# Kernel optimization log

Hardware: AMD Instinct MI355X
Metric: run time of the kernel (lower is better)

Reference implementation:

```python
import jax, jax.numpy as jnp
import numpy as np

B, T, N, D = 32, 50, 100, 4
E = N * (N - 1)
N_IN, N_HID, N_OUT = T * D, 256, 4


def _mlp(x, w1, b1, w2, b2):
    # Linear -> ReLU -> (dropout=0) -> Linear
    return jax.nn.relu(x @ w1 + b1) @ w2 + b2


def setup_inputs() -> dict:
    key = jax.random.key(0)
    ks = jax.random.split(key, 12)
    # fully-connected directed graph, no self loops
    idx = np.array([(i, j) for i in range(N) for j in range(N) if i != j], dtype=np.int64)
    recv, sendr = idx[:, 0], idx[:, 1]
    rec = jnp.asarray(np.eye(N, dtype=np.float32)[recv])    # [E, N]
    send = jnp.asarray(np.eye(N, dtype=np.float32)[sendr])  # [E, N]

    def lin(k, fan_in, fan_out):
        kw, kb = jax.random.split(k)
        w = jax.random.normal(kw, (fan_in, fan_out), jnp.float32) * 0.02
        b = jax.random.normal(kb, (fan_out,), jnp.float32) * 0.02
        return w, b

    x = jax.random.normal(ks[0], (B, T, N, D), jnp.float32)
    w1a, b1a = lin(ks[1], N_IN, N_HID)
    w1b, b1b = lin(ks[2], N_HID, N_HID)
    w2a, b2a = lin(ks[3], 2 * N_HID, N_HID)
    w2b, b2b = lin(ks[4], N_HID, N_HID)
    w3a, b3a = lin(ks[5], N_HID, N_HID)
    w3b, b3b = lin(ks[6], N_HID, N_HID)
    w4a, b4a = lin(ks[7], 3 * N_HID, N_HID)
    w4b, b4b = lin(ks[8], N_HID, N_HID)
    wo, bo = lin(ks[9], N_HID, N_OUT)
    return {"x": x, "rec": rec, "send": send,
            "w1a": w1a, "b1a": b1a, "w1b": w1b, "b1b": b1b,
            "w2a": w2a, "b2a": b2a, "w2b": w2b, "b2b": b2b,
            "w3a": w3a, "b3a": b3a, "w3b": w3b, "b3b": b3b,
            "w4a": w4a, "b4a": b4a, "w4b": w4b, "b4b": b4b,
            "wo": wo, "bo": bo}


def reference(x, rec, send,
              w1a, b1a, w1b, b1b,
              w2a, b2a, w2b, b2b,
              w3a, b3a, w3b, b3b,
              w4a, b4a, w4b, b4b,
              wo, bo):
    # [B, T, N, D] -> [B, N, T*D]
    h = jnp.transpose(x, (0, 2, 1, 3)).reshape(x.shape[0], x.shape[2], -1)
    h = _mlp(h, w1a, b1a, w1b, b1b)                       # [B, N, H]
    # v2e: gather receiver/sender node states to edges
    e = jnp.concatenate([jnp.einsum('en,bnh->beh', rec, h),
                         jnp.einsum('en,bnh->beh', send, h)], axis=2)  # [B, E, 2H]
    e = _mlp(e, w2a, b2a, w2b, b2b)                       # [B, E, H]
    x_skip = e
    # e2v: scatter edges back to nodes, normalize by n_nodes
    v = jnp.einsum('en,beh->bnh', rec, e) / e.shape[-2] * (e.shape[-2] / rec.shape[1])
    v = jnp.einsum('en,beh->bnh', rec, e) / rec.shape[1]  # incoming / incoming.size(1)=N
    v = _mlp(v, w3a, b3a, w3b, b3b)                       # [B, N, H]
    e2 = jnp.concatenate([jnp.einsum('en,bnh->beh', rec, v),
                          jnp.einsum('en,bnh->beh', send, v)], axis=2)  # [B, E, 2H]
    e2 = jnp.concatenate([e2, x_skip], axis=2)            # [B, E, 3H]
    e2 = _mlp(e2, w4a, b4a, w4b, b4b)                     # [B, E, H]
    return e2 @ wo + bo                                   # [B, E, n_out]
```

## Files before the change

kernel.cpp:

```cpp
#include <hip/hip_runtime.h>
#include <hip/hip_bf16.h>
#include <stdint.h>


typedef __attribute__((ext_vector_type(8))) short short8;
typedef __attribute__((ext_vector_type(4))) float float4v;
typedef __attribute__((ext_vector_type(4))) unsigned short ushort4v;

__device__ inline float bf2f(unsigned short u) {
    union { unsigned int i; float f; } v; v.i = ((unsigned int)u) << 16; return v.f;
}

#if __has_builtin(__builtin_amdgcn_cvt_pk_bf16_f32)
typedef __attribute__((ext_vector_type(2))) __bf16 bf16x2;
__device__ inline unsigned int f2bf_pk(float a, float b) {
    union { bf16x2 v; unsigned int u; } c;
    c.v = __builtin_amdgcn_cvt_pk_bf16_f32(a, b);
    return c.u;
}
__device__ inline unsigned short f2bf(float f) {
    return (unsigned short)(f2bf_pk(f, f) & 0xFFFFu);
}
#else
__device__ inline unsigned short f2bf(float f) {
    union { float f; unsigned int i; } v; v.f = f;
    unsigned int i = v.i;
    return (unsigned short)((i + 0x7FFFu + ((i >> 16) & 1u)) >> 16);
}
__device__ inline unsigned int f2bf_pk(float a, float b) {
    return (unsigned int)f2bf(a) | ((unsigned int)f2bf(b) << 16);
}
#endif

__global__ __launch_bounds__(256) void prep_kernel(
        const float* __restrict__ x,
        const float* __restrict__ w1a, const float* __restrict__ w1b,
        const float* __restrict__ w2a, const float* __restrict__ w2b,
        const float* __restrict__ w3a, const float* __restrict__ w3b,
        const float* __restrict__ w4a, const float* __restrict__ b4a,
        const float* __restrict__ w4b, const float* __restrict__ b4b,
        const float* __restrict__ wo,  const float* __restrict__ bo,
        const float* __restrict__ b2b,
        unsigned short* __restrict__ Wp1a, unsigned short* __restrict__ Wp1b,
        unsigned short* __restrict__ Wp2r, unsigned short* __restrict__ Wp2s,
        unsigned short* __restrict__ Wp2b, unsigned short* __restrict__ Wp3a,
        unsigned short* __restrict__ Wp3b, unsigned short* __restrict__ Wp4r,
        unsigned short* __restrict__ Wp4s, unsigned short* __restrict__ Wpz,
        unsigned short* __restrict__ Wfp, float* __restrict__ bfv,
        float* __restrict__ b4ap, float* __restrict__ b2bs,
        unsigned short* __restrict__ hin) {
    int bx = blockIdx.x;
    int tid = threadIdx.x;
    if (bx < 2272) {
        const float* W; unsigned short* Wp; int Kin; int b0;
        if      (bx <  224) { W = w1a;             Wp = Wp1a; Kin = 200; b0 = 0;    }
        else if (bx <  480) { W = w1b;             Wp = Wp1b; Kin = 256; b0 = 224;  }
        else if (bx <  736) { W = w2a;             Wp = Wp2r; Kin = 256; b0 = 480;  }
        else if (bx <  992) { W = w2a + 256 * 256; Wp = Wp2s; Kin = 256; b0 = 736;  }
        else if (bx < 1248) { W = w2b;             Wp = Wp2b; Kin = 256; b0 = 992;  }
        else if (bx < 1504) { W = w3a;             Wp = Wp3a; Kin = 256; b0 = 1248; }
        else if (bx < 1760) { W = w3b;             Wp = Wp3b; Kin = 256; b0 = 1504; }
        else if (bx < 2016) { W = w4a;             Wp = Wp4r; Kin = 256; b0 = 1760; }
        else                { W = w4a + 256 * 256; Wp = Wp4s; Kin = 256; b0 = 2016; }
        int idx = (bx - b0) * 256 + tid;
        int k = idx >> 8, n = idx & 255;
        unsigned short v = (k < Kin) ? f2bf(W[k * 256 + n]) : (unsigned short)0;
        Wp[((size_t)(k >> 5) * 256 + n) * 32 + (k & 31)] = v;
    } else if (bx < 2528) {
        int k = bx - 2272, c = tid;
        float s = 0.f;
        for (int t = 0; t < 256; ++t)
            s += w2b[k * 256 + t] * w4a[(size_t)(512 + t) * 256 + c];
        Wpz[((size_t)(k >> 5) * 256 + c) * 32 + (k & 31)] = f2bf(s);
    } else if (bx < 2530) {
        int k = tid;
        if (bx == 2528) {
            float a[4] = {0.f, 0.f, 0.f, 0.f};
            for (int c = 0; c < 256; ++c) {
                float wv = w4b[k * 256 + c];
                #pragma unroll
                for (int o = 0; o < 4; ++o) a[o] += wv * wo[c * 4 + o];
            }
            #pragma unroll
            for (int n = 0; n < 16; ++n)
                Wfp[(size_t)(k >> 5) * 512 + n * 32 + (k & 31)] =
                    (n < 4) ? f2bf(a[n]) : (unsigned short)0;
            if (k < 4) {
                float s = bo[k];
                for (int c = 0; c < 256; ++c) s += b4b[c] * wo[c * 4 + k];
                bfv[k] = s;
            }
        } else {
            float s = b4a[k];
            for (int t = 0; t < 256; ++t)
                s += b2b[t] * w4a[(size_t)(512 + t) * 256 + k];
            b4ap[k] = s;
            b2bs[k] = 0.99f * b2b[k];
        }
    } else {
        int idx = (bx - 2530) * 256 + tid;
        if (idx < 3200 * 224) {
            int row = idx / 224;
            int c = idx - row * 224;
            int b = row / 100, n = row - b * 100;
            unsigned short v = 0;
            if (c < 200) {
                int t = c >> 2, d = c & 3;
                v = f2bf(x[(((size_t)(b * 50 + t)) * 100 + n) * 4 + d]);
            }
            hin[(size_t)row * 224 + c] = v;
        }
    }
}

__global__ __launch_bounds__(256) void node_fusedA_kernel(
        const unsigned short* __restrict__ hin,
        const unsigned short* __restrict__ Wp1a, const float* __restrict__ b1a,
        const unsigned short* __restrict__ Wp1b, const float* __restrict__ b1b,
        const unsigned short* __restrict__ Wp2r, const float* __restrict__ b2a,
        const unsigned short* __restrict__ Wp2s,
        unsigned short* __restrict__ U, unsigned short* __restrict__ Hs) {
    __shared__ __align__(16) unsigned short t1s[16 * 264];
    __shared__ __align__(16) unsigned short hs2[16 * 264];
    const int m0 = blockIdx.x * 16;
    const int tid  = threadIdx.x;
    const int wave = tid >> 6;
    const int lane = tid & 63;
    const int l15  = lane & 15;
    const int quad = lane >> 4;
    const int n0   = wave * 64;
    const int koff = quad * 8;

    {
        float4v acc[4];
        #pragma unroll
        for (int ni = 0; ni < 4; ++ni) acc[ni] = (float4v)(0.0f);
        for (int kb = 0; kb < 7; ++kb) {
            short8 af = *(const short8*)(hin + (size_t)(m0 + l15) * 224 + kb * 32 + koff);
            short8 bf[4];
            #pragma unroll
            for (int ni = 0; ni < 4; ++ni)
                bf[ni] = *(const short8*)(Wp1a + ((size_t)kb * 256 + n0 + ni * 16 + l15) * 32 + koff);
            #pragma unroll
            for (int ni = 0; ni < 4; ++ni)
                acc[ni] = __builtin_amdgcn_mfma_f32_16x16x32_bf16(af, bf[ni], acc[ni], 0, 0, 0);
        }
        #pragma unroll
        for (int ni = 0; ni < 4; ++ni) {
            int col = n0 + ni * 16 + l15;
            float bv = b1a[col];
            #pragma unroll
            for (int r = 0; r < 4; ++r) {
                float v = acc[ni][r] + bv;
                v = v > 0.f ? v : 0.f;
                t1s[(quad * 4 + r) * 264 + col] = f2bf(v);
            }
        }
    }
    __syncthreads();

    {
        float4v acc[4];
        #pragma unroll
        for (int ni = 0; ni < 4; ++ni) acc[ni] = (float4v)(0.0f);
        for (int kb = 0; kb < 8; ++kb) {
            short8 af = *(const short8*)(&t1s[l15 * 264 + kb * 32 + koff]);
            short8 bf[4];
            #pragma unroll
            for (int ni = 0; ni < 4; ++ni)
                bf[ni] = *(const short8*)(Wp1b + ((size_t)kb * 256 + n0 + ni * 16 + l15) * 32 + koff);
            #pragma unroll
            for (int ni = 0; ni < 4; ++ni)
                acc[ni] = __builtin_amdgcn_mfma_f32_16x16x32_bf16(af, bf[ni], acc[ni], 0, 0, 0);
        }
        #pragma unroll
        for (int ni = 0; ni < 4; ++ni) {
            int col = n0 + ni * 16 + l15;
            float bv = b1b[col];
            #pragma unroll
            for (int r = 0; r < 4; ++r)
                hs2[(quad * 4 + r) * 264 + col] = f2bf(acc[ni][r] + bv);
        }
    }
    __syncthreads();

    {
        float4v aU[4], aH[4];
        #pragma unroll
        for (int ni = 0; ni < 4; ++ni) { aU[ni] = (float4v)(0.0f); aH[ni] = (float4v)(0.0f); }
        for (int kb = 0; kb < 8; ++kb) {
            short8 af = *(const short8*)(&hs2[l15 * 264 + kb * 32 + koff]);
            #pragma unroll
            for (int ni = 0; ni < 4; ++ni) {
                short8 bu = *(const short8*)(Wp2r + ((size_t)kb * 256 + n0 + ni * 16 + l15) * 32 + koff);
                short8 bh = *(const short8*)(Wp2s + ((size_t)kb * 256 + n0 + ni * 16 + l15) * 32 + koff);
                aU[ni] = __builtin_amdgcn_mfma_f32_16x16x32_bf16(af, bu, aU[ni], 0, 0, 0);
                aH[ni] = __builtin_amdgcn_mfma_f32_16x16x32_bf16(af, bh, aH[ni], 0, 0, 0);
            }
        }
        #pragma unroll
        for (int ni = 0; ni < 4; ++ni) {
            int col = n0 + ni * 16 + l15;
            float bv = b2a[col];
            #pragma unroll
            for (int r = 0; r < 4; ++r) {
                size_t o = (size_t)(m0 + quad * 4 + r) * 256 + col;
                U[o]  = f2bf(aU[ni][r] + bv);
                Hs[o] = f2bf(aH[ni][r]);
            }
        }
    }
}

__global__ __launch_bounds__(256) void node_fusedC_kernel(
        const unsigned short* __restrict__ Ssc,
        const unsigned short* __restrict__ Wp2b, const float* __restrict__ b2bs,
        const unsigned short* __restrict__ Wp3a, const float* __restrict__ b3a,
        const unsigned short* __restrict__ Wp3b, const float* __restrict__ b3b,
        const unsigned short* __restrict__ Wp4r, const float* __restrict__ b4ap,
        const unsigned short* __restrict__ Wp4s,
        unsigned short* __restrict__ C4, unsigned short* __restrict__ Vs) {
    __shared__ __align__(16) unsigned short buf0[16 * 264];
    __shared__ __align__(16) unsigned short buf1[16 * 264];
    const int m0 = blockIdx.x * 16;
    const int tid  = threadIdx.x;
    const int wave = tid >> 6;
    const int lane = tid & 63;
    const int l15  = lane & 15;
    const int quad = lane >> 4;
    const int n0   = wave * 64;
    const int koff = quad * 8;

    {
        float4v acc[4];
        #pragma unroll
        for (int ni = 0; ni < 4; ++ni) acc[ni] = (float4v)(0.0f);
        for (int kb = 0; kb < 8; ++kb) {
            short8 af = *(const short8*)(Ssc + (size_t)(m0 + l15) * 256 + kb * 32 + koff);
            short8 bf[4];
            #pragma unroll
            for (int ni = 0; ni < 4; ++ni)
                bf[ni] = *(const short8*)(Wp2b + ((size_t)kb * 256 + n0 + ni * 16 + l15) * 32 + koff);
            #pragma unroll
            for (int ni = 0; ni < 4; ++ni)
                acc[ni] = __builtin_amdgcn_mfma_f32_16x16x32_bf16(af, bf[ni], acc[ni], 0, 0, 0);
        }
        #pragma unroll
        for (int ni = 0; ni < 4; ++ni) {
            int col = n0 + ni * 16 + l15;
            float bv = b2bs[col];
            #pragma unroll
            for (int r = 0; r < 4; ++r)
                buf0[(quad * 4 + r) * 264 + col] = f2bf(acc[ni][r] + bv);
        }
    }
    __syncthreads();

    {
        float4v acc[4];
        #pragma unroll
        for (int ni = 0; ni < 4; ++ni) acc[ni] = (float4v)(0.0f);
        for (int kb = 0; kb < 8; ++kb) {
            short8 af = *(const short8*)(&buf0[l15 * 264 + kb * 32 + koff]);
            short8 bf[4];
            #pragma unroll
            for (int ni = 0; ni < 4; ++ni)
                bf[ni] = *(const short8*)(Wp3a + ((size_t)kb * 256 + n0 + ni * 16 + l15) * 32 + koff);
            #pragma unroll
            for (int ni = 0; ni < 4; ++ni)
                acc[ni] = __builtin_amdgcn_mfma_f32_16x16x32_bf16(af, bf[ni], acc[ni], 0, 0, 0);
        }
        #pragma unroll
        for (int ni = 0; ni < 4; ++ni) {
            int col = n0 + ni * 16 + l15;
            float bv = b3a[col];
            #pragma unroll
            for (int r = 0; r < 4; ++r) {
                float v = acc[ni][r] + bv;
                v = v > 0.f ? v : 0.f;
                buf1[(quad * 4 + r) * 264 + col] = f2bf(v);
            }
        }
    }
    __syncthreads();

    {
        float4v acc[4];
        #pragma unroll
        for (int ni = 0; ni < 4; ++ni) acc[ni] = (float4v)(0.0f);
        for (int kb = 0; kb < 8; ++kb) {
            short8 af = *(const short8*)(&buf1[l15 * 264 + kb * 32 + koff]);
            short8 bf[4];
            #pragma unroll
            for (int ni = 0; ni < 4; ++ni)
                bf[ni] = *(const short8*)(Wp3b + ((size_t)kb * 256 + n0 + ni * 16 + l15) * 32 + koff);
            #pragma unroll
            for (int ni = 0; ni < 4; ++ni)
                acc[ni] = __builtin_amdgcn_mfma_f32_16x16x32_bf16(af, bf[ni], acc[ni], 0, 0, 0);
        }
        __syncthreads();
        #pragma unroll
        for (int ni = 0; ni < 4; ++ni) {
            int col = n0 + ni * 16 + l15;
            float bv = b3b[col];
            #pragma unroll
            for (int r = 0; r < 4; ++r)
                buf0[(quad * 4 + r) * 264 + col] = f2bf(acc[ni][r] + bv);
        }
    }
    __syncthreads();

    {
        float4v aC[4], aV[4];
        #pragma unroll
        for (int ni = 0; ni < 4; ++ni) { aC[ni] = (float4v)(0.0f); aV[ni] = (float4v)(0.0f); }
        for (int kb = 0; kb < 8; ++kb) {
            short8 af = *(const short8*)(&buf0[l15 * 264 + kb * 32 + koff]);
            #pragma unroll
            for (int ni = 0; ni < 4; ++ni) {
                short8 bc = *(const short8*)(Wp4r + ((size_t)kb * 256 + n0 + ni * 16 + l15) * 32 + koff);
                short8 bv = *(const short8*)(Wp4s + ((size_t)kb * 256 + n0 + ni * 16 + l15) * 32 + koff);
                aC[ni] = __builtin_amdgcn_mfma_f32_16x16x32_bf16(af, bc, aC[ni], 0, 0, 0);
                aV[ni] = __builtin_amdgcn_mfma_f32_16x16x32_bf16(af, bv, aV[ni], 0, 0, 0);
            }
        }
        #pragma unroll
        for (int ni = 0; ni < 4; ++ni) {
            int col = n0 + ni * 16 + l15;
            float bv = b4ap[col];
            #pragma unroll
            for (int r = 0; r < 4; ++r) {
                size_t o = (size_t)(m0 + quad * 4 + r) * 256 + col;
                C4[o] = f2bf(aC[ni][r] + bv);
                Vs[o] = f2bf(aV[ni][r]);
            }
        }
    }
}

__global__ __launch_bounds__(256) void colsum_kernel(
        const unsigned short* __restrict__ U, const unsigned short* __restrict__ Hs,
        unsigned short* __restrict__ Ssc) {
    const int g = blockIdx.x;
    const int b = g / 100, i = g - b * 100;
    const int c = threadIdx.x;
    const float u = bf2f(U[(size_t)g * 256 + c]);
    const unsigned short* base = Hs + (size_t)b * 100 * 256 + c;
    float s = 0.f;
    #pragma unroll 4
    for (int j = 0; j < 100; ++j) {
        float v = u + bf2f(base[(size_t)j * 256]);
        s += (v > 0.f ? v : 0.f);
    }
    float vi = u + bf2f(base[(size_t)i * 256]);
    s -= (vi > 0.f ? vi : 0.f);
    Ssc[(size_t)g * 256 + c] = f2bf(s * 0.01f);
}

__global__ __launch_bounds__(256, 4) void edge_phaseB_kernel(
        const unsigned short* __restrict__ Hs, const unsigned short* __restrict__ Vs,
        const unsigned short* __restrict__ U, const unsigned short* __restrict__ C4,
        const unsigned short* __restrict__ Wpz, const unsigned short* __restrict__ Wfp,
        const float* __restrict__ bfv,
        float* __restrict__ out) {
    __shared__ __align__(16) unsigned short t2s[64 * 264];
    const int g = blockIdx.x, hb = blockIdx.y;
    const int b = g / 100, nr = g - b * 100;
    const int nrows = hb ? 49 : 50;
    const int k0 = hb * 50;
    const int tid  = threadIdx.x;
    const int wave = tid >> 6;
    const int lane = tid & 63;
    const int l15  = lane & 15;
    const int quad = lane >> 4;
    const int n0   = wave * 64;
    const int koff = quad * 8;

    {
        const int c = lane * 4;
        ushort4v uv = *(const ushort4v*)(U + (size_t)g * 256 + c);
        float u0 = bf2f(uv[0]), u1 = bf2f(uv[1]), u2 = bf2f(uv[2]), u3 = bf2f(uv[3]);
        for (int r = wave; r < 64; r += 4) {
            unsigned int p01 = 0, p23 = 0;
            if (r < nrows) {
                int k = k0 + r;
                int j = k + (k >= nr ? 1 : 0);
                ushort4v hv = *(const ushort4v*)(Hs + (size_t)(b * 100 + j) * 256 + c);
                float t0 = u0 + bf2f(hv[0]); t0 = t0 > 0.f ? t0 : 0.f;
                float t1 = u1 + bf2f(hv[1]); t1 = t1 > 0.f ? t1 : 0.f;
                float t2 = u2 + bf2f(hv[2]); t2 = t2 > 0.f ? t2 : 0.f;
                float t3 = u3 + bf2f(hv[3]); t3 = t3 > 0.f ? t3 : 0.f;
                p01 = f2bf_pk(t0, t1);
                p23 = f2bf_pk(t2, t3);
            }
            unsigned int* dst = (unsigned int*)(&t2s[r * 264 + c]);
            dst[0] = p01;
            dst[1] = p23;
        }
    }
    __syncthreads();

    float4v acc[4][4];
    #pragma unroll
    for (int mi = 0; mi < 4; ++mi)
        #pragma unroll
        for (int ni = 0; ni < 4; ++ni) acc[mi][ni] = (float4v)(0.0f);

    #pragma unroll 1
    for (int kb = 0; kb < 8; ++kb) {
        short8 af[4], bf[4];
        #pragma unroll
        for (int mi = 0; mi < 4; ++mi)
            af[mi] = *(const short8*)(&t2s[(mi * 16 + l15) * 264 + kb * 32 + koff]);
        #pragma unroll
        for (int ni = 0; ni < 4; ++ni)
            bf[ni] = *(const short8*)(Wpz + ((size_t)kb * 256 + n0 + ni * 16 + l15) * 32 + koff);
        #pragma unroll
        for (int mi = 0; mi < 4; ++mi)
            #pragma unroll
            for (int ni = 0; ni < 4; ++ni)
                acc[mi][ni] = __builtin_amdgcn_mfma_f32_16x16x32_bf16(af[mi], bf[ni], acc[mi][ni], 0, 0, 0);
    }
    __syncthreads();

    float c4v[4];
    #pragma unroll
    for (int ni = 0; ni < 4; ++ni)
        c4v[ni] = bf2f(C4[(size_t)g * 256 + n0 + ni * 16 + l15]);
    #pragma unroll
    for (int mi = 0; mi < 4; ++mi) {
        #pragma unroll
        for (int r = 0; r < 4; ++r) {
            int row = mi * 16 + quad * 4 + r;
            int k = k0 + row;
            int j = (row < nrows) ? (k + (k >= nr ? 1 : 0)) : 0;
            const unsigned short* vsr = Vs + (size_t)(b * 100 + j) * 256;
            #pragma unroll
            for (int ni = 0; ni < 4; ++ni) {
                int col = n0 + ni * 16 + l15;
                float zv = c4v[ni] + bf2f(vsr[col]) + acc[mi][ni][r];
                zv = zv > 0.f ? zv : 0.f;
                t2s[row * 264 + col] = f2bf(zv);
            }
        }
    }
    __syncthreads();

    float4v pacc = (float4v)(0.0f);
    #pragma unroll
    for (int kb = 0; kb < 8; ++kb) {
        short8 za = *(const short8*)(&t2s[(wave * 16 + l15) * 264 + kb * 32 + koff]);
        short8 wb = *(const short8*)(Wfp + (size_t)kb * 512 + l15 * 32 + koff);
        pacc = __builtin_amdgcn_mfma_f32_16x16x32_bf16(za, wb, pacc, 0, 0, 0);
    }

    if (l15 < 4) {
        float bv = bfv[l15];
        #pragma unroll
        for (int r = 0; r < 4; ++r) {
            int row = wave * 16 + quad * 4 + r;
            if (row < nrows)
                out[((size_t)b * 9900 + nr * 99 + k0 + row) * 4 + l15] = pacc[r] + bv;
        }
    }
}

extern "C" void kernel_launch(void* const* d_in, const int* in_sizes, int n_in,
                              void* d_out, int out_size, void* d_ws, size_t ws_size,
                              hipStream_t stream) {
    const float* x   = (const float*)d_in[0];
    const float* w1a = (const float*)d_in[3];
    const float* b1a = (const float*)d_in[4];
    const float* w1b = (const float*)d_in[5];
    const float* b1b = (const float*)d_in[6];
    const float* w2a = (const float*)d_in[7];
    const float* b2a = (const float*)d_in[8];
    const float* w2b = (const float*)d_in[9];
    const float* b2b = (const float*)d_in[10];
    const float* w3a = (const float*)d_in[11];
    const float* b3a = (const float*)d_in[12];
    const float* w3b = (const float*)d_in[13];
    const float* b3b = (const float*)d_in[14];
    const float* w4a = (const float*)d_in[15];
    const float* b4a = (const float*)d_in[16];
    const float* w4b = (const float*)d_in[17];
    const float* b4b = (const float*)d_in[18];
    const float* wo  = (const float*)d_in[19];
    const float* bo  = (const float*)d_in[20];
    float* out = (float*)d_out;
    (void)in_sizes; (void)n_in; (void)out_size; (void)ws_size;

    char* ws = (char*)d_ws;
    size_t off = 0;
    auto alloc = [&](size_t bytes) {
        size_t o = off;
        off = (off + bytes + 255) & ~(size_t)255;
        return o;
    };
    const size_t SLOT_BF = (size_t)3200 * 256 * 2;
    unsigned short* S_U  = (unsigned short*)(ws + alloc(SLOT_BF));
    unsigned short* S_Hs = (unsigned short*)(ws + alloc(SLOT_BF));
    unsigned short* S_Vs = (unsigned short*)(ws + alloc(SLOT_BF));
    unsigned short* S_4  = (unsigned short*)(ws + alloc(SLOT_BF));
    unsigned short* Wp1a = (unsigned short*)(ws + alloc(224 * 256 * 2));
    unsigned short* Wp1b = (unsigned short*)(ws + alloc(256 * 256 * 2));
    unsigned short* Wp2r = (unsigned short*)(ws + alloc(256 * 256 * 2));
    unsigned short* Wp2s = (unsigned short*)(ws + alloc(256 * 256 * 2));
    unsigned short* Wp2b = (unsigned short*)(ws + alloc(256 * 256 * 2));
    unsigned short* Wp3a = (unsigned short*)(ws + alloc(256 * 256 * 2));
    unsigned short* Wp3b = (unsigned short*)(ws + alloc(256 * 256 * 2));
    unsigned short* Wp4r = (unsigned short*)(ws + alloc(256 * 256 * 2));
    unsigned short* Wp4s = (unsigned short*)(ws + alloc(256 * 256 * 2));
    unsigned short* Wpz  = (unsigned short*)(ws + alloc(256 * 256 * 2));
    unsigned short* Wfp  = (unsigned short*)(ws + alloc(8 * 16 * 32 * 2));
    float*          bfv  = (float*)(ws + alloc(4 * 4));
    float*          b4ap = (float*)(ws + alloc(256 * 4));
    float*          b2bs = (float*)(ws + alloc(256 * 4));

    unsigned short* hin = S_4;
    unsigned short* Ssc = S_4;
    unsigned short* C4  = S_4;

    hipLaunchKernelGGL(prep_kernel, dim3(5330), dim3(256), 0, stream,
                       x, w1a, w1b, w2a, w2b, w3a, w3b, w4a, b4a, w4b, b4b, wo, bo, b2b,
                       Wp1a, Wp1b, Wp2r, Wp2s, Wp2b, Wp3a, Wp3b, Wp4r, Wp4s, Wpz,
                       Wfp, bfv, b4ap, b2bs, hin);
    hipLaunchKernelGGL(node_fusedA_kernel, dim3(200), dim3(256), 0, stream,
                       hin, Wp1a, b1a, Wp1b, b1b, Wp2r, b2a, Wp2s, S_U, S_Hs);
    hipLaunchKernelGGL(colsum_kernel, dim3(3200), dim3(256), 0, stream, S_U, S_Hs, Ssc);
    hipLaunchKernelGGL(node_fusedC_kernel, dim3(200), dim3(256), 0, stream,
                       Ssc, Wp2b, b2bs, Wp3a, b3a, Wp3b, b3b, Wp4r, b4ap, Wp4s, C4, S_Vs);
    hipLaunchKernelGGL(edge_phaseB_kernel, dim3(3200, 2), dim3(256), 0, stream,
                       S_Hs, S_Vs, S_U, C4, Wpz, Wfp, bfv, out);
}
```

Before: 267.9 us.

## Split edge_phaseB work across eight waves per block instead of four

The edge_phaseB kernel now runs with 512 threads, so each wave owns 32 output columns instead of 64 in the main MFMA GEMM. The staging loop and the ReLU/store epilogue are repartitioned to match. The final small projection runs only on the first four waves. The aim is to cut per-wave register use and serial MFMA chain length and to raise wave-level parallelism. The cost is that each A fragment is loaded from LDS by twice as many waves, and half the waves sit idle in the last stage.

Result: faster. 259.6 us (-3.1%).

```diff
diff --git a/kernel.cpp b/kernel.cpp
--- a/kernel.cpp
+++ b/kernel.cpp
@@ -357,7 +357,7 @@
     Ssc[(size_t)g * 256 + c] = f2bf(s * 0.01f);
 }
 
-__global__ __launch_bounds__(256, 4) void edge_phaseB_kernel(
+__global__ __launch_bounds__(512, 6) void edge_phaseB_kernel(
         const unsigned short* __restrict__ Hs, const unsigned short* __restrict__ Vs,
         const unsigned short* __restrict__ U, const unsigned short* __restrict__ C4,
         const unsigned short* __restrict__ Wpz, const unsigned short* __restrict__ Wfp,
@@ -373,14 +373,14 @@
     const int lane = tid & 63;
     const int l15  = lane & 15;
     const int quad = lane >> 4;
-    const int n0   = wave * 64;
+    const int n0   = wave * 32;
     const int koff = quad * 8;
 
     {
         const int c = lane * 4;
         ushort4v uv = *(const ushort4v*)(U + (size_t)g * 256 + c);
         float u0 = bf2f(uv[0]), u1 = bf2f(uv[1]), u2 = bf2f(uv[2]), u3 = bf2f(uv[3]);
-        for (int r = wave; r < 64; r += 4) {
+        for (int r = wave; r < 64; r += 8) {
             unsigned int p01 = 0, p23 = 0;
             if (r < nrows) {
                 int k = k0 + r;
@@ -400,67 +400,64 @@
     }
     __syncthreads();
 
-    float4v acc[4][4];
+    float4v acc[4][2];
     #pragma unroll
-    for (int mi = 0; mi < 4; ++mi)
-        #pragma unroll
-        for (int ni = 0; ni < 4; ++ni) acc[mi][ni] = (float4v)(0.0f);
+    for (int mi = 0; mi < 4; ++mi) {
+        acc[mi][0] = (float4v)(0.0f);
+        acc[mi][1] = (float4v)(0.0f);
+    }
 
     #pragma unroll 1
     for (int kb = 0; kb < 8; ++kb) {
-        short8 af[4], bf[4];
-        #pragma unroll
-        for (int mi = 0; mi < 4; ++mi)
-            af[mi] = *(const short8*)(&t2s[(mi * 16 + l15) * 264 + kb * 32 + koff]);
-        #pragma unroll
-        for (int ni = 0; ni < 4; ++ni)
-            bf[ni] = *(const short8*)(Wpz + ((size_t)kb * 256 + n0 + ni * 16 + l15) * 32 + koff);
-        #pragma unroll
-        for (int mi = 0; mi < 4; ++mi)
-            #pragma unroll
-            for (int ni = 0; ni < 4; ++ni)
-                acc[mi][ni] = __builtin_amdgcn_mfma_f32_16x16x32_bf16(af[mi], bf[ni], acc[mi][ni], 0, 0, 0);
-    }
-    __syncthreads();
-
-    float c4v[4];
-    #pragma unroll
-    for (int ni = 0; ni < 4; ++ni)
-        c4v[ni] = bf2f(C4[(size_t)g * 256 + n0 + ni * 16 + l15]);
-    #pragma unroll
-    for (int mi = 0; mi < 4; ++mi) {
-        #pragma unroll
-        for (int r = 0; r < 4; ++r) {
-            int row = mi * 16 + quad * 4 + r;
-            int k = k0 + row;
-            int j = (row < nrows) ? (k + (k >= nr ? 1 : 0)) : 0;
-            const unsigned short* vsr = Vs + (size_t)(b * 100 + j) * 256;
-            #pragma unroll
-            for (int ni = 0; ni < 4; ++ni) {
-                int col = n0 + ni * 16 + l15;
-                float zv = c4v[ni] + bf2f(vsr[col]) + acc[mi][ni][r];
-                zv = zv > 0.f ? zv : 0.f;
-                t2s[row * 264 + col] = f2bf(zv);
-            }
-        }
-    }
-    __syncthreads();
-
-    float4v pacc = (float4v)(0.0f);
-    #pragma unroll
-    for (int kb = 0; kb < 8; ++kb) {
-        short8 za = *(const short8*)(&t2s[(wave * 16 + l15) * 264 + kb * 32 + koff]);
-        short8 wb = *(const short8*)(Wfp + (size_t)kb * 512 + l15 * 32 + koff);
-        pacc = __builtin_amdgcn_mfma_f32_16x16x32_bf16(za, wb, pacc, 0, 0, 0);
-    }
-
-    if (l15 < 4) {
-        float bv = bfv[l15];
-        #pragma unroll
-        for (int r = 0; r < 4; ++r) {
-            int row = wave * 16 + quad * 4 + r;
-            if (row < nrows)
-                out[((size_t)b * 9900 + nr * 99 + k0 + row) * 4 + l15] = pacc[r] + bv;
+        short8 bf0 = *(const short8*)(Wpz + ((size_t)kb * 256 + n0 + l15) * 32 + koff);
+        short8 bf1 = *(const short8*)(Wpz + ((size_t)kb * 256 + n0 + 16 + l15) * 32 + koff);
+        #pragma unroll
+        for (int mi = 0; mi < 4; ++mi) {
+            short8 af = *(const short8*)(&t2s[(mi * 16 + l15) * 264 + kb * 32 + koff]);
+            acc[mi][0] = __builtin_amdgcn_mfma_f32_16x16x32_bf16(af, bf0, acc[mi][0], 0, 0, 0);
+            acc[mi][1] = __builtin_amdgcn_mfma_f32_16x16x32_bf16(af, bf1, acc[mi][1], 0, 0, 0);
+        }
+    }
+    __syncthreads();
+
+    {
+        float c4v0 = bf2f(C4[(size_t)g * 256 + n0 + l15]);
+        float c4v1 = bf2f(C4[(size_t)g * 256 + n0 + 16 + l15]);
+        #pragma unroll
+        for (int mi = 0; mi < 4; ++mi) {
+            #pragma unroll
+            for (int r = 0; r < 4; ++r) {
+                int row = mi * 16 + quad * 4 + r;
+                int k = k0 + row;
+                int j = (row < nrows) ? (k + (k >= nr ? 1 : 0)) : 0;
+                const unsigned short* vsr = Vs + (size_t)(b * 100 + j) * 256;
+                float z0 = c4v0 + bf2f(vsr[n0 + l15]) + acc[mi][0][r];
+                float z1 = c4v1 + bf2f(vsr[n0 + 16 + l15]) + acc[mi][1][r];
+                z0 = z0 > 0.f ? z0 : 0.f;
+                z1 = z1 > 0.f ? z1 : 0.f;
+                t2s[row * 264 + n0 + l15]      = f2bf(z0);
+                t2s[row * 264 + n0 + 16 + l15] = f2bf(z1);
+            }
+        }
+    }
+    __syncthreads();
+
+    if (wave < 4) {
+        float4v pacc = (float4v)(0.0f);
+        #pragma unroll
+        for (int kb = 0; kb < 8; ++kb) {
+            short8 za = *(const short8*)(&t2s[(wave * 16 + l15) * 264 + kb * 32 + koff]);
+            short8 wb = *(const short8*)(Wfp + (size_t)kb * 512 + l15 * 32 + koff);
+            pacc = __builtin_amdgcn_mfma_f32_16x16x32_bf16(za, wb, pacc, 0, 0, 0);
+        }
+        if (l15 < 4) {
+            float bv = bfv[l15];
+            #pragma unroll
+            for (int r = 0; r < 4; ++r) {
+                int row = wave * 16 + quad * 4 + r;
+                if (row < nrows)
+                    out[((size_t)b * 9900 + nr * 99 + k0 + row) * 4 + l15] = pacc[r] + bv;
+            }
         }
     }
 }
@@ -530,6 +527,6 @@
     hipLaunchKernelGGL(colsum_kernel, dim3(3200), dim3(256), 0, stream, S_U, S_Hs, Ssc);
     hipLaunchKernelGGL(node_fusedC_kernel, dim3(200), dim3(256), 0, stream,
                        Ssc, Wp2b, b2bs, Wp3a, b3a, Wp3b, b3b, Wp4r, b4ap, Wp4s, C4, S_Vs);
-    hipLaunchKernelGGL(edge_phaseB_kernel, dim3(3200, 2), dim3(256), 0, stream,
+    hipLaunchKernelGGL(edge_phaseB_kernel, dim3(3200, 2), dim3(512), 0, stream,
                        S_Hs, S_Vs, S_U, C4, Wpz, Wfp, bfv, out);
 }
```
